# Kernel optimization log

Measured on AMD Instinct MI355X. Metric: run time of the kernel, lower is better.

Reference implementation:

```python
import jax, jax.numpy as jnp
import numpy as np

B, N, HID, EPOCH = 16, 512, 32, 201


def setup_inputs() -> dict:
    key = jax.random.key(0)
    k1, k2, k3, k4 = jax.random.split(key, 4)
    f = jax.random.normal(k1, (B, 1, N, N), dtype=jnp.float32)
    # per-sample 3x3 stencil: perturbed 5-point Laplacian, positive center for stable Jacobi
    base = jnp.array([[0., -1., 0.], [-1., 4., -1.], [0., -1., 0.]], dtype=jnp.float32)
    kernelA = base[None, None] + 0.1 * jax.random.normal(k2, (B, 1, 3, 3), dtype=jnp.float32)
    kernelA = kernelA.at[:, :, 1, 1].set(jnp.maximum(kernelA[:, :, 1, 1], 1.0))
    u = jnp.zeros((B, 1, N, N), jnp.float32)
    # stand-in DeepONet H: pointwise 2 -> HID -> 1 MLP on concat(LFA, residual)
    W1 = 0.1 * jax.random.normal(k3, (HID, 2), dtype=jnp.float32)
    b1 = jnp.zeros((HID,), jnp.float32)
    W2 = 0.1 * jax.random.normal(k4, (1, HID), dtype=jnp.float32)
    b2 = jnp.zeros((1,), jnp.float32)
    return {"f": f, "kernelA": kernelA, "u": u, "W1": W1, "b1": b1, "W2": W2, "b2": b2, "epoch": EPOCH}


def _A(x, kernel):
    # per-sample 3x3 stencil: batch dim mapped to channels, grouped conv (groups = B)
    bsz = x.shape[0]
    y = jax.lax.conv_general_dilated(
        jnp.transpose(x, (1, 0, 2, 3)), kernel, (1, 1), ((1, 1), (1, 1)),
        dimension_numbers=("NCHW", "OIHW", "NCHW"), feature_group_count=bsz)
    return jnp.transpose(y, (1, 0, 2, 3))


def _lfa(kernelA, n):
    # ComputeSmootherFactor: Jacobi symbol |prod_j (1 - tau * A_hat(theta))| on the frequency grid
    h = 1.0 / (n + 1)
    p = np.arange(-(n // 2), n // 2)
    P1, P2 = np.meshgrid(p, p)
    t1 = jnp.asarray(2j * np.pi * h * P1, jnp.complex64)
    t2 = jnp.asarray(2j * np.pi * h * P2, jnp.complex64)
    E = jnp.stack([
        jnp.exp(-t1 - t2), jnp.exp(-t2), jnp.exp(t1 - t2),
        jnp.exp(-t1), jnp.ones_like(t1), jnp.exp(t1),
        jnp.exp(-t1 + t2), jnp.exp(t2), jnp.exp(t1 + t2)])  # [9,N,N]
    bsz = kernelA.shape[0]
    S = jnp.einsum("bk,kxy->bxy", kernelA.reshape(bsz, 9).astype(jnp.complex64), E)
    tau = (0.5 / kernelA[:, 0, 1, 1]).astype(jnp.complex64)[:, None, None]
    y = (1.0 - tau * S) ** 5  # 5 identical Jacobi factors
    return jnp.abs(y)[:, None].astype(jnp.float32)  # [B,1,N,N]


def _H(lfa, r, W1, b1, W2, b2):
    # pointwise MLP correction operator (stand-in for DeepONet)
    z = jnp.concatenate([lfa, r], axis=1)  # [B,2,N,N]
    hdn = jax.nn.gelu(jnp.einsum("bcxy,oc->boxy", z, W1) + b1[None, :, None, None])
    return jnp.einsum("bcxy,oc->boxy", hdn, W2) + b2[None, :, None, None]


def reference(f, kernelA, u, W1, b1, W2, b2, epoch):
    K = (epoch - 1) // 100 + 1
    n = f.shape[-1]
    lfa = _lfa(kernelA, n)
    taus = 0.5 / kernelA[:, :, 1:2, 1:2]  # [B,1,1,1], w=0.5
    x = jnp.zeros_like(f)
    for _ in range(K):
        for _ in range(10):  # jacobi, M=10
            x = x + taus * (f - _A(x, kernelA))
        r = f - _A(x, kernelA)
        x = x + _H(lfa, r, W1, b1, W2, b2)
    r = f - _A(x, kernelA)
    return jnp.linalg.norm(r) / jnp.linalg.norm(f)
```

## Files before the change

kernel.cpp:

```cpp
#include <hip/hip_runtime.h>
#include <math.h>

#define BB 16
#define NN 512
#define HID 32

#define HALO 16
#define TW 96
#define TWP 97
#define OT 64

#define GELU_K1 (-2.302208201f)
#define GELU_K2 (-0.102944244f)

#define TPH 0.012247925f
#define CDR 0.99992499f
#define SDR 0.012247618f

__global__ __launch_bounds__(256) void lfa_kernel(const float* __restrict__ kernelA,
                                                  float* __restrict__ lfa) {
    const int t = threadIdx.x;
    const int strip = t & 127;
    const int i = blockIdx.y * 2 + (t >> 7);
    const int b = blockIdx.z;
    const int j0 = strip * 4;
    const float* a = kernelA + b * 9;
    float a0 = a[0], a1 = a[1], a2 = a[2], a3 = a[3], a4 = a[4];
    float a5 = a[5], a6 = a[6], a7 = a[7], a8 = a[8];
    const float A35 = a3 + a5, A17 = a1 + a7, A08 = a0 + a8, A26 = a2 + a6;
    const float B53 = a5 - a3, B71 = a7 - a1, B80 = a8 - a0, B26 = a2 - a6;
    const float tau = 0.5f / a4;

    float th2 = TPH * (float)(i - NN / 2);
    float th1 = TPH * (float)(j0 - NN / 2);
    float s1, c1, s2, c2;
    sincosf(th1, &s1, &c1);
    sincosf(th2, &s2, &c2);

    float out[4];
#pragma unroll
    for (int k = 0; k < 4; ++k) {
        float cc = c1 * c2, ss = s1 * s2, sc = s1 * c2, cs = c1 * s2;
        float cpp = cc - ss, cpm = cc + ss, spp = sc + cs, spm = sc - cs;
        float re = fmaf(A35, c1, a4); re = fmaf(A17, c2, re);
        re = fmaf(A08, cpp, re);      re = fmaf(A26, cpm, re);
        float im = B53 * s1;          im = fmaf(B71, s2, im);
        im = fmaf(B80, spp, im);      im = fmaf(B26, spm, im);
        float zre = fmaf(-tau, re, 1.0f);
        float zim = tau * im;
        float m2 = fmaf(zre, zre, zim * zim);
        out[k] = m2 * m2 * sqrtf(m2);
        float tt = s1 * SDR;
        float ns = fmaf(s1, CDR, c1 * SDR);
        c1 = fmaf(c1, CDR, -tt);
        s1 = ns;
    }
    float4 ov = {out[0], out[1], out[2], out[3]};
    *(float4*)(lfa + (size_t)b * NN * NN + (size_t)i * NN + j0) = ov;
}

template <bool FIRST>
__global__ __launch_bounds__(256) void fused_cycle(
        const float* __restrict__ xin, float* __restrict__ xout,
        const float* __restrict__ f, const float* __restrict__ kernelA,
        const float* __restrict__ lfa,
        const float* __restrict__ W1, const float* __restrict__ b1,
        const float* __restrict__ W2, const float* __restrict__ b2) {
    __shared__ float sxraw[98 * TWP + 2];
    float* sx = sxraw + TWP + 1;
    const int tx = threadIdx.x;
    const int ty = threadIdx.y;
    const int t  = ty * 32 + tx;
    const int b  = blockIdx.z;
    const int gy0 = blockIdx.y * OT;
    const int gx0 = blockIdx.x * OT;
    const int goi = gy0 - HALO;
    const int goj = gx0 - HALO;
    const float* fg = f + (size_t)b * NN * NN;
    const float* ag = kernelA + b * 9;
    const float ar0 = ag[0], ar1 = ag[1], ar2 = ag[2], ar3 = ag[3], ar4 = ag[4];
    const float ar5 = ag[5], ar6 = ag[6], ar7 = ag[7], ar8 = ag[8];
    const float tau = 0.5f / ar4;
    const float s0 = tau * ar0, q1 = tau * ar1, q2 = tau * ar2, q3 = tau * ar3;
    const float q4 = tau * ar4, q5 = tau * ar5, q6 = tau * ar6, q7 = tau * ar7;
    const float q8 = tau * ar8;

    if (t < 98) sxraw[t] = 0.f;
    if (t < 96) sxraw[97 + 97 * t] = 0.f;
    if (t < 98) sxraw[9409 + t] = 0.f;

    if (!FIRST) {
        const float* xg = xin + (size_t)b * NN * NN;
#pragma unroll
        for (int k = 0; k < (TW * TW) / 256; ++k) {
            int idx = t + k * 256;
            int row = idx / TW, col = idx - row * TW;
            int gi = goi + row, gj = goj + col;
            float v = 0.f;
            if (gi >= 0 && gi < NN && gj >= 0 && gj < NN) v = xg[gi * NN + gj];
            sx[row * TWP + col] = v;
        }
    }

    const int R0 = ty * 12, C0 = tx * 3;

    const float* pb  = sx + (R0 - 1) * TWP + (C0 - 1);
    float*       pwv = sx + R0 * TWP + C0;

    float vR[12], vC[3];
#pragma unroll
    for (int r = 0; r < 12; ++r) {
        int R = R0 + r, gi = goi + R;
        vR[r] = (R >= 1 && R < TW - 1 && gi >= 0 && gi < NN) ? 1.f : 0.f;
    }
#pragma unroll
    for (int c = 0; c < 3; ++c) {
        int C = C0 + c, gj = goj + C;
        vC[c] = (C >= 1 && C < TW - 1 && gj >= 0 && gj < NN) ? 1.f : 0.f;
    }

    float frt[12][3];
#pragma unroll
    for (int r = 0; r < 12; ++r) {
        int gi = goi + R0 + r;
#pragma unroll
        for (int c = 0; c < 3; ++c) {
            int gj = goj + C0 + c;
            frt[r][c] = (gi >= 0 && gi < NN && gj >= 0 && gj < NN)
                            ? tau * fg[gi * NN + gj] : 0.f;
        }
    }

    __syncthreads();

    float cur[12][3];
    if (FIRST) {
#pragma unroll
        for (int r = 0; r < 12; ++r) {
#pragma unroll
            for (int c = 0; c < 3; ++c)
                cur[r][c] = (vR[r] * vC[c]) * frt[r][c];
        }
        pwv[0] = cur[0][0]; pwv[1] = cur[0][1]; pwv[2] = cur[0][2];
        pwv[11 * TWP] = cur[11][0]; pwv[11 * TWP + 1] = cur[11][1];
        pwv[11 * TWP + 2] = cur[11][2];
#pragma unroll
        for (int r = 1; r < 11; ++r) {
            pwv[r * TWP] = cur[r][0];
            pwv[r * TWP + 2] = cur[r][2];
        }
        __syncthreads();
    } else {
#pragma unroll
        for (int r = 0; r < 12; ++r) {
            cur[r][0] = pwv[r * TWP];
            cur[r][1] = pwv[r * TWP + 1];
            cur[r][2] = pwv[r * TWP + 2];
        }
    }

    for (int s = FIRST ? 1 : 0; s < 10; ++s) {
        float top0 = pb[0], top1 = pb[1], top2 = pb[2], top3 = pb[3], top4 = pb[4];
        float bot0 = pb[13 * TWP],     bot1 = pb[13 * TWP + 1],
              bot2 = pb[13 * TWP + 2], bot3 = pb[13 * TWP + 3],
              bot4 = pb[13 * TWP + 4];
        float pm0 = top1, pm1v = top2, pm2 = top3;
        float Lm1 = top0, Rm1 = top4;
        float Lc = pb[TWP], Rc = pb[TWP + 4];
#pragma unroll
        for (int r = 0; r < 12; ++r) {
            float n0, n1, n2, Lp, Rp;
            if (r < 11) {
                n0 = cur[r + 1][0]; n1 = cur[r + 1][1]; n2 = cur[r + 1][2];
                Lp = pb[(r + 2) * TWP];
                Rp = pb[(r + 2) * TWP + 4];
            } else {
                n0 = bot1; n1 = bot2; n2 = bot3; Lp = bot0; Rp = bot4;
            }
            float o0 = cur[r][0], o1 = cur[r][1], o2 = cur[r][2];
            {
                float ax = s0 * Lm1;
                ax = fmaf(q1, pm0, ax); ax = fmaf(q2, pm1v, ax);
                ax = fmaf(q3, Lc, ax);  ax = fmaf(q4, o0, ax);
                ax = fmaf(q5, o1, ax);  ax = fmaf(q6, Lp, ax);
                ax = fmaf(q7, n0, ax);  ax = fmaf(q8, n1, ax);
                cur[r][0] = fmaf(vR[r] * vC[0], frt[r][0] - ax, o0);
            }
            {
                float ax = s0 * pm0;
                ax = fmaf(q1, pm1v, ax); ax = fmaf(q2, pm2, ax);
                ax = fmaf(q3, o0, ax);   ax = fmaf(q4, o1, ax);
                ax = fmaf(q5, o2, ax);   ax = fmaf(q6, n0, ax);
                ax = fmaf(q7, n1, ax);   ax = fmaf(q8, n2, ax);
                cur[r][1] = fmaf(vR[r] * vC[1], frt[r][1] - ax, o1);
            }
            {
                float ax = s0 * pm1v;
                ax = fmaf(q1, pm2, ax); ax = fmaf(q2, Rm1, ax);
                ax = fmaf(q3, o1, ax);  ax = fmaf(q4, o2, ax);
                ax = fmaf(q5, Rc, ax);  ax = fmaf(q6, n1, ax);
                ax = fmaf(q7, n2, ax);  ax = fmaf(q8, Rp, ax);
                cur[r][2] = fmaf(vR[r] * vC[2], frt[r][2] - ax, o2);
            }
            pm0 = o0; pm1v = o1; pm2 = o2;
            Lm1 = Lc; Rm1 = Rc; Lc = Lp; Rc = Rp;
        }
        __syncthreads();
        if (s < 9) {
            pwv[0] = cur[0][0]; pwv[1] = cur[0][1]; pwv[2] = cur[0][2];
            pwv[11 * TWP] = cur[11][0]; pwv[11 * TWP + 1] = cur[11][1];
            pwv[11 * TWP + 2] = cur[11][2];
#pragma unroll
            for (int r = 1; r < 11; ++r) {
                pwv[r * TWP] = cur[r][0];
                pwv[r * TWP + 2] = cur[r][2];
            }
        } else {
#pragma unroll
            for (int r = 0; r < 12; ++r) {
                pwv[r * TWP] = cur[r][0];
                pwv[r * TWP + 1] = cur[r][1];
                pwv[r * TWP + 2] = cur[r][2];
            }
        }
        __syncthreads();
    }

    const int orow = t >> 2;
    const int oseg = t & 3;
    const int Rl = HALO + orow;
    const int Cl0 = HALO + oseg * 16;
    const float* pw = sx + (Rl - 1) * TWP + (Cl0 - 1);
    float w0[18], w1[18], w2[18];
#pragma unroll
    for (int k = 0; k < 18; ++k) {
        w0[k] = pw[k];
        w1[k] = pw[TWP + k];
        w2[k] = pw[2 * TWP + k];
    }
    const int gi = gy0 + orow;
    const int gjb = gx0 + oseg * 16;
    const float4* f4 = (const float4*)(fg + (size_t)gi * NN + gjb);
    const float4* l4 = (const float4*)(lfa + (size_t)b * NN * NN + (size_t)gi * NN + gjb);
    float fv[16], lv[16];
#pragma unroll
    for (int q = 0; q < 4; ++q) {
        float4 fq = f4[q], lq = l4[q];
        fv[q * 4] = fq.x; fv[q * 4 + 1] = fq.y; fv[q * 4 + 2] = fq.z; fv[q * 4 + 3] = fq.w;
        lv[q * 4] = lq.x; lv[q * 4 + 1] = lq.y; lv[q * 4 + 2] = lq.z; lv[q * 4 + 3] = lq.w;
    }
    float rv[16];
#pragma unroll
    for (int k = 0; k < 16; ++k) {
        float ax = ar0 * w0[k];
        ax = fmaf(ar1, w0[k + 1], ax); ax = fmaf(ar2, w0[k + 2], ax);
        ax = fmaf(ar3, w1[k], ax);     ax = fmaf(ar4, w1[k + 1], ax);
        ax = fmaf(ar5, w1[k + 2], ax); ax = fmaf(ar6, w2[k], ax);
        ax = fmaf(ar7, w2[k + 1], ax); ax = fmaf(ar8, w2[k + 2], ax);
        rv[k] = fv[k] - ax;
    }
    float acc[16];
#pragma unroll
    for (int k = 0; k < 16; ++k) acc[k] = 0.f;
    for (int hh = 0; hh < HID; ++hh) {
        float w1a = W1[2 * hh], w1b = W1[2 * hh + 1], bb = b1[hh], wo = W2[hh];
#pragma unroll
        for (int k = 0; k < 16; ++k) {
            float v = fmaf(w1a, lv[k], fmaf(w1b, rv[k], bb));
            float m = v * fmaf(GELU_K2, v * v, GELU_K1);
            float e = __builtin_amdgcn_exp2f(m);
            float g = v * __builtin_amdgcn_rcpf(1.0f + e);
            acc[k] = fmaf(wo, g, acc[k]);
        }
    }
    const float b2v = b2[0];
    float4* xo4 = (float4*)(xout + (size_t)b * NN * NN + (size_t)gi * NN + gjb);
#pragma unroll
    for (int q = 0; q < 4; ++q) {
        float4 ov;
        ov.x = w1[q * 4 + 1] + acc[q * 4] + b2v;
        ov.y = w1[q * 4 + 2] + acc[q * 4 + 1] + b2v;
        ov.z = w1[q * 4 + 3] + acc[q * 4 + 2] + b2v;
        ov.w = w1[q * 4 + 4] + acc[q * 4 + 3] + b2v;
        xo4[q] = ov;
    }
}

__global__ __launch_bounds__(256) void resnorm_kernel(const float* __restrict__ xin,
                                                      const float* __restrict__ f,
                                                      const float* __restrict__ kernelA,
                                                      float* __restrict__ acc) {
    const int total_strips = BB * NN * (NN / 4);
    float rr = 0.f, f2 = 0.f;
    for (int p = blockIdx.x * 256 + threadIdx.x; p < total_strips;
         p += gridDim.x * 256) {
        int b = p >> 16;
        int rem = p & 65535;
        int i = rem >> 7;
        int js = (rem & 127) << 2;
        const float* a = kernelA + b * 9;
        const float* x = xin + (size_t)b * NN * NN;

        float4 up = {0,0,0,0}, mid, dn = {0,0,0,0};
        float upl = 0.f, upr = 0.f, midl = 0.f, midr = 0.f, dnl = 0.f, dnr = 0.f;
        const float* rowm = x + (size_t)i * NN + js;
        mid = *(const float4*)rowm;
        if (js > 0)       midl = rowm[-1];
        if (js + 4 < NN)  midr = rowm[4];
        if (i > 0) {
            const float* rowu = rowm - NN;
            up = *(const float4*)rowu;
            if (js > 0)      upl = rowu[-1];
            if (js + 4 < NN) upr = rowu[4];
        }
        if (i + 1 < NN) {
            const float* rowd = rowm + NN;
            dn = *(const float4*)rowd;
            if (js > 0)      dnl = rowd[-1];
            if (js + 4 < NN) dnr = rowd[4];
        }
        float u[6] = {upl, up.x, up.y, up.z, up.w, upr};
        float m[6] = {midl, mid.x, mid.y, mid.z, mid.w, midr};
        float d[6] = {dnl, dn.x, dn.y, dn.z, dn.w, dnr};
        float4 fq = *(const float4*)(f + (size_t)b * NN * NN + (size_t)i * NN + js);
        float fvv[4] = {fq.x, fq.y, fq.z, fq.w};
#pragma unroll
        for (int c = 0; c < 4; ++c) {
            float ax = a[0] * u[c];
            ax = fmaf(a[1], u[c + 1], ax); ax = fmaf(a[2], u[c + 2], ax);
            ax = fmaf(a[3], m[c], ax);     ax = fmaf(a[4], m[c + 1], ax);
            ax = fmaf(a[5], m[c + 2], ax); ax = fmaf(a[6], d[c], ax);
            ax = fmaf(a[7], d[c + 1], ax); ax = fmaf(a[8], d[c + 2], ax);
            float r = fvv[c] - ax;
            rr = fmaf(r, r, rr);
            f2 = fmaf(fvv[c], fvv[c], f2);
        }
    }
#pragma unroll
    for (int off = 32; off > 0; off >>= 1) {
        rr += __shfl_down(rr, off, 64);
        f2 += __shfl_down(f2, off, 64);
    }
    __shared__ float sr[4], sf[4];
    int wave = threadIdx.x >> 6;
    if ((threadIdx.x & 63) == 0) { sr[wave] = rr; sf[wave] = f2; }
    __syncthreads();
    if (threadIdx.x == 0) {
        atomicAdd(&acc[0], sr[0] + sr[1] + sr[2] + sr[3]);
        atomicAdd(&acc[1], sf[0] + sf[1] + sf[2] + sf[3]);
    }
}

__global__ void finalize_kernel(const float* __restrict__ acc, float* __restrict__ out) {
    out[0] = sqrtf(acc[0] / acc[1]);
}

extern "C" void kernel_launch(void* const* d_in, const int* in_sizes, int n_in,
                              void* d_out, int out_size, void* d_ws, size_t ws_size,
                              hipStream_t stream) {
    const float* f  = (const float*)d_in[0];
    const float* kA = (const float*)d_in[1];
    float*       u  = (float*)d_in[2];
    const float* W1 = (const float*)d_in[3];
    const float* b1 = (const float*)d_in[4];
    const float* W2 = (const float*)d_in[5];
    const float* b2 = (const float*)d_in[6];
    float* out = (float*)d_out;

    char* ws = (char*)d_ws;
    float* acc = (float*)ws;
    float* xB  = (float*)(ws + 256);
    float* lfa = (float*)(ws + 256 + (size_t)BB * NN * NN * 4);

    hipMemsetAsync(acc, 0, 2 * sizeof(float), stream);

    lfa_kernel<<<dim3(1, NN / 2, BB), 256, 0, stream>>>(kA, lfa);

    dim3 jblk(32, 8);
    dim3 jgrd(NN / OT, NN / OT, BB);

    fused_cycle<true><<<jgrd, jblk, 0, stream>>>(u, xB, f, kA, lfa, W1, b1, W2, b2);
    fused_cycle<false><<<jgrd, jblk, 0, stream>>>(xB, u, f, kA, lfa, W1, b1, W2, b2);
    fused_cycle<false><<<jgrd, jblk, 0, stream>>>(u, xB, f, kA, lfa, W1, b1, W2, b2);

    resnorm_kernel<<<2048, 256, 0, stream>>>(xB, f, kA, acc);
    finalize_kernel<<<1, 1, 0, stream>>>(acc, out);
}
```

Baseline: 431.1 us.

## Fuse LFA computation and final residual norm into the cycle kernels

Folds the LFA symbol computation into the first fused cycle kernel, with each block computing its own tile, and zeroes the accumulator there instead of through a memset. The last cycle no longer writes x to global memory. It stages the H correction in shared memory, recomputes it on a one-cell ring of halo points, and computes the final residual and norms in-kernel. This removes the separate LFA, memset and resnorm launches plus a full write and read of x. The cost is redundant MLP work on the ring points, extra barriers, and a launch-bounds hint that may limit registers.

```diff
diff --git a/kernel.cpp b/kernel.cpp
--- a/kernel.cpp
+++ b/kernel.cpp
@@ -17,55 +17,14 @@
 #define CDR 0.99992499f
 #define SDR 0.012247618f
 
-__global__ __launch_bounds__(256) void lfa_kernel(const float* __restrict__ kernelA,
-                                                  float* __restrict__ lfa) {
-    const int t = threadIdx.x;
-    const int strip = t & 127;
-    const int i = blockIdx.y * 2 + (t >> 7);
-    const int b = blockIdx.z;
-    const int j0 = strip * 4;
-    const float* a = kernelA + b * 9;
-    float a0 = a[0], a1 = a[1], a2 = a[2], a3 = a[3], a4 = a[4];
-    float a5 = a[5], a6 = a[6], a7 = a[7], a8 = a[8];
-    const float A35 = a3 + a5, A17 = a1 + a7, A08 = a0 + a8, A26 = a2 + a6;
-    const float B53 = a5 - a3, B71 = a7 - a1, B80 = a8 - a0, B26 = a2 - a6;
-    const float tau = 0.5f / a4;
-
-    float th2 = TPH * (float)(i - NN / 2);
-    float th1 = TPH * (float)(j0 - NN / 2);
-    float s1, c1, s2, c2;
-    sincosf(th1, &s1, &c1);
-    sincosf(th2, &s2, &c2);
-
-    float out[4];
-#pragma unroll
-    for (int k = 0; k < 4; ++k) {
-        float cc = c1 * c2, ss = s1 * s2, sc = s1 * c2, cs = c1 * s2;
-        float cpp = cc - ss, cpm = cc + ss, spp = sc + cs, spm = sc - cs;
-        float re = fmaf(A35, c1, a4); re = fmaf(A17, c2, re);
-        re = fmaf(A08, cpp, re);      re = fmaf(A26, cpm, re);
-        float im = B53 * s1;          im = fmaf(B71, s2, im);
-        im = fmaf(B80, spp, im);      im = fmaf(B26, spm, im);
-        float zre = fmaf(-tau, re, 1.0f);
-        float zim = tau * im;
-        float m2 = fmaf(zre, zre, zim * zim);
-        out[k] = m2 * m2 * sqrtf(m2);
-        float tt = s1 * SDR;
-        float ns = fmaf(s1, CDR, c1 * SDR);
-        c1 = fmaf(c1, CDR, -tt);
-        s1 = ns;
-    }
-    float4 ov = {out[0], out[1], out[2], out[3]};
-    *(float4*)(lfa + (size_t)b * NN * NN + (size_t)i * NN + j0) = ov;
-}
-
-template <bool FIRST>
-__global__ __launch_bounds__(256) void fused_cycle(
+template <bool FIRST, bool RES>
+__global__ __launch_bounds__(256, 4) void fused_cycle(
         const float* __restrict__ xin, float* __restrict__ xout,
         const float* __restrict__ f, const float* __restrict__ kernelA,
-        const float* __restrict__ lfa,
+        float* __restrict__ lfa,
         const float* __restrict__ W1, const float* __restrict__ b1,
-        const float* __restrict__ W2, const float* __restrict__ b2) {
+        const float* __restrict__ W2, const float* __restrict__ b2,
+        float* __restrict__ accp) {
     __shared__ float sxraw[98 * TWP + 2];
     float* sx = sxraw + TWP + 1;
     const int tx = threadIdx.x;
@@ -85,6 +44,48 @@
     const float q4 = tau * ar4, q5 = tau * ar5, q6 = tau * ar6, q7 = tau * ar7;
     const float q8 = tau * ar8;
 
+    if (FIRST) {
+        if (t == 0 && (blockIdx.x | blockIdx.y | blockIdx.z) == 0) {
+            accp[0] = 0.f;
+            accp[1] = 0.f;
+        }
+        const int orw = t >> 2;
+        const int osg = t & 3;
+        const int gi_ = gy0 + orw;
+        const int gj_ = gx0 + osg * 16;
+        const float A35 = ar3 + ar5, A17 = ar1 + ar7, A08 = ar0 + ar8, A26 = ar2 + ar6;
+        const float B53 = ar5 - ar3, B71 = ar7 - ar1, B80 = ar8 - ar0, B26 = ar2 - ar6;
+        float th2 = TPH * (float)(gi_ - NN / 2);
+        float s2v, c2v;
+        sincosf(th2, &s2v, &c2v);
+        float* lrow = lfa + (size_t)b * NN * NN + (size_t)gi_ * NN + gj_;
+        for (int g = 0; g < 4; ++g) {
+            float th1 = TPH * (float)(gj_ + g * 4 - NN / 2);
+            float s1, c1;
+            sincosf(th1, &s1, &c1);
+            float out[4];
+#pragma unroll
+            for (int k = 0; k < 4; ++k) {
+                float cc = c1 * c2v, ss = s1 * s2v, sc = s1 * c2v, cs = c1 * s2v;
+                float cpp = cc - ss, cpm = cc + ss, spp = sc + cs, spm = sc - cs;
+                float re = fmaf(A35, c1, ar4); re = fmaf(A17, c2v, re);
+                re = fmaf(A08, cpp, re);       re = fmaf(A26, cpm, re);
+                float im = B53 * s1;           im = fmaf(B71, s2v, im);
+                im = fmaf(B80, spp, im);       im = fmaf(B26, spm, im);
+                float zre = fmaf(-tau, re, 1.0f);
+                float zim = tau * im;
+                float m2 = fmaf(zre, zre, zim * zim);
+                out[k] = m2 * m2 * sqrtf(m2);
+                float tt = s1 * SDR;
+                float ns = fmaf(s1, CDR, c1 * SDR);
+                c1 = fmaf(c1, CDR, -tt);
+                s1 = ns;
+            }
+            float4 ov = {out[0], out[1], out[2], out[3]};
+            *(float4*)(lrow + g * 4) = ov;
+        }
+    }
+
     if (t < 98) sxraw[t] = 0.f;
     if (t < 96) sxraw[97 + 97 * t] = 0.f;
     if (t < 98) sxraw[9409 + t] = 0.f;
@@ -259,6 +260,12 @@
         ax = fmaf(ar7, w2[k + 1], ax); ax = fmaf(ar8, w2[k + 2], ax);
         rv[k] = fv[k] - ax;
     }
+    float f2 = 0.f;
+    if (RES) {
+#pragma unroll
+        for (int k = 0; k < 16; ++k) f2 = fmaf(fv[k], fv[k], f2);
+    }
+    const float b2v = b2[0];
     float acc[16];
 #pragma unroll
     for (int k = 0; k < 16; ++k) acc[k] = 0.f;
@@ -273,81 +280,106 @@
             acc[k] = fmaf(wo, g, acc[k]);
         }
     }
-    const float b2v = b2[0];
-    float4* xo4 = (float4*)(xout + (size_t)b * NN * NN + (size_t)gi * NN + gjb);
-#pragma unroll
-    for (int q = 0; q < 4; ++q) {
-        float4 ov;
-        ov.x = w1[q * 4 + 1] + acc[q * 4] + b2v;
-        ov.y = w1[q * 4 + 2] + acc[q * 4 + 1] + b2v;
-        ov.z = w1[q * 4 + 3] + acc[q * 4 + 2] + b2v;
-        ov.w = w1[q * 4 + 4] + acc[q * 4 + 3] + b2v;
-        xo4[q] = ov;
-    }
-}
-
-__global__ __launch_bounds__(256) void resnorm_kernel(const float* __restrict__ xin,
-                                                      const float* __restrict__ f,
-                                                      const float* __restrict__ kernelA,
-                                                      float* __restrict__ acc) {
-    const int total_strips = BB * NN * (NN / 4);
-    float rr = 0.f, f2 = 0.f;
-    for (int p = blockIdx.x * 256 + threadIdx.x; p < total_strips;
-         p += gridDim.x * 256) {
-        int b = p >> 16;
-        int rem = p & 65535;
-        int i = rem >> 7;
-        int js = (rem & 127) << 2;
-        const float* a = kernelA + b * 9;
-        const float* x = xin + (size_t)b * NN * NN;
-
-        float4 up = {0,0,0,0}, mid, dn = {0,0,0,0};
-        float upl = 0.f, upr = 0.f, midl = 0.f, midr = 0.f, dnl = 0.f, dnr = 0.f;
-        const float* rowm = x + (size_t)i * NN + js;
-        mid = *(const float4*)rowm;
-        if (js > 0)       midl = rowm[-1];
-        if (js + 4 < NN)  midr = rowm[4];
-        if (i > 0) {
-            const float* rowu = rowm - NN;
-            up = *(const float4*)rowu;
-            if (js > 0)      upl = rowu[-1];
-            if (js + 4 < NN) upr = rowu[4];
-        }
-        if (i + 1 < NN) {
-            const float* rowd = rowm + NN;
-            dn = *(const float4*)rowd;
-            if (js > 0)      dnl = rowd[-1];
-            if (js + 4 < NN) dnr = rowd[4];
-        }
-        float u[6] = {upl, up.x, up.y, up.z, up.w, upr};
-        float m[6] = {midl, mid.x, mid.y, mid.z, mid.w, midr};
-        float d[6] = {dnl, dn.x, dn.y, dn.z, dn.w, dnr};
-        float4 fq = *(const float4*)(f + (size_t)b * NN * NN + (size_t)i * NN + js);
-        float fvv[4] = {fq.x, fq.y, fq.z, fq.w};
-#pragma unroll
-        for (int c = 0; c < 4; ++c) {
-            float ax = a[0] * u[c];
-            ax = fmaf(a[1], u[c + 1], ax); ax = fmaf(a[2], u[c + 2], ax);
-            ax = fmaf(a[3], m[c], ax);     ax = fmaf(a[4], m[c + 1], ax);
-            ax = fmaf(a[5], m[c + 2], ax); ax = fmaf(a[6], d[c], ax);
-            ax = fmaf(a[7], d[c + 1], ax); ax = fmaf(a[8], d[c + 2], ax);
-            float r = fvv[c] - ax;
+
+    if (RES) {
+        float Hr0 = 0.f, Hr1 = 0.f;
+        int hoff0 = 0, hoff1 = 0;
+        auto ringH = [&](int rc, float& Hv, int& hoff) {
+            int R, C;
+            if (rc < 66)       { R = 15; C = 15 + rc; }
+            else if (rc < 132) { R = 80; C = rc - 51; }
+            else if (rc < 196) { R = rc - 116; C = 15; }
+            else               { R = rc - 180; C = 80; }
+            hoff = R * TWP + C;
+            int rgi = goi + R, rgj = goj + C;
+            Hv = 0.f;
+            if (rgi >= 0 && rgi < NN && rgj >= 0 && rgj < NN) {
+                const float* pr = sx + (R - 1) * TWP + (C - 1);
+                float u0 = pr[0], u1 = pr[1], u2 = pr[2];
+                float m0 = pr[TWP], m1 = pr[TWP + 1], m2 = pr[TWP + 2];
+                float d0 = pr[2 * TWP], d1 = pr[2 * TWP + 1], d2 = pr[2 * TWP + 2];
+                float ax = ar0 * u0;
+                ax = fmaf(ar1, u1, ax); ax = fmaf(ar2, u2, ax);
+                ax = fmaf(ar3, m0, ax); ax = fmaf(ar4, m1, ax);
+                ax = fmaf(ar5, m2, ax); ax = fmaf(ar6, d0, ax);
+                ax = fmaf(ar7, d1, ax); ax = fmaf(ar8, d2, ax);
+                float rp = fg[(size_t)rgi * NN + rgj] - ax;
+                float lf = lfa[(size_t)b * NN * NN + (size_t)rgi * NN + rgj];
+                float av = 0.f;
+                for (int hh = 0; hh < HID; ++hh) {
+                    float w1a = W1[2 * hh], w1b = W1[2 * hh + 1], bbv = b1[hh], wo = W2[hh];
+                    float v = fmaf(w1a, lf, fmaf(w1b, rp, bbv));
+                    float m = v * fmaf(GELU_K2, v * v, GELU_K1);
+                    float e = __builtin_amdgcn_exp2f(m);
+                    float gg = v * __builtin_amdgcn_rcpf(1.0f + e);
+                    av = fmaf(wo, gg, av);
+                }
+                Hv = av + b2v;
+            }
+        };
+        ringH(t, Hr0, hoff0);
+        if (t < 4) ringH(t + 256, Hr1, hoff1);
+
+        __syncthreads();
+        float* ph = sx + Rl * TWP + Cl0;
+#pragma unroll
+        for (int k = 0; k < 16; ++k) ph[k] = acc[k] + b2v;
+        sx[hoff0] = Hr0;
+        if (t < 4) sx[hoff1] = Hr1;
+        __syncthreads();
+
+        float hr[18];
+#pragma unroll
+        for (int k = 0; k < 18; ++k) hr[k] = pw[k];
+#pragma unroll
+        for (int k = 0; k < 16; ++k) {
+            float ax = ar0 * hr[k];
+            ax = fmaf(ar1, hr[k + 1], ax);
+            ax = fmaf(ar2, hr[k + 2], ax);
+            rv[k] -= ax;
+        }
+#pragma unroll
+        for (int k = 0; k < 18; ++k) hr[k] = pw[TWP + k];
+#pragma unroll
+        for (int k = 0; k < 16; ++k) {
+            float ax = ar3 * hr[k];
+            ax = fmaf(ar4, hr[k + 1], ax);
+            ax = fmaf(ar5, hr[k + 2], ax);
+            rv[k] -= ax;
+        }
+#pragma unroll
+        for (int k = 0; k < 18; ++k) hr[k] = pw[2 * TWP + k];
+        float rr = 0.f;
+#pragma unroll
+        for (int k = 0; k < 16; ++k) {
+            float ax = ar6 * hr[k];
+            ax = fmaf(ar7, hr[k + 1], ax);
+            ax = fmaf(ar8, hr[k + 2], ax);
+            float r = rv[k] - ax;
             rr = fmaf(r, r, rr);
-            f2 = fmaf(fvv[c], fvv[c], f2);
-        }
-    }
-#pragma unroll
-    for (int off = 32; off > 0; off >>= 1) {
-        rr += __shfl_down(rr, off, 64);
-        f2 += __shfl_down(f2, off, 64);
-    }
-    __shared__ float sr[4], sf[4];
-    int wave = threadIdx.x >> 6;
-    if ((threadIdx.x & 63) == 0) { sr[wave] = rr; sf[wave] = f2; }
-    __syncthreads();
-    if (threadIdx.x == 0) {
-        atomicAdd(&acc[0], sr[0] + sr[1] + sr[2] + sr[3]);
-        atomicAdd(&acc[1], sf[0] + sf[1] + sf[2] + sf[3]);
+        }
+#pragma unroll
+        for (int off = 32; off > 0; off >>= 1) {
+            rr += __shfl_down(rr, off, 64);
+            f2 += __shfl_down(f2, off, 64);
+        }
+        if ((t & 63) == 0) { sxraw[t >> 6] = rr; sxraw[4 + (t >> 6)] = f2; }
+        __syncthreads();
+        if (t == 0) {
+            atomicAdd(&accp[0], sxraw[0] + sxraw[1] + sxraw[2] + sxraw[3]);
+            atomicAdd(&accp[1], sxraw[4] + sxraw[5] + sxraw[6] + sxraw[7]);
+        }
+    } else {
+        float4* xo4 = (float4*)(xout + (size_t)b * NN * NN + (size_t)gi * NN + gjb);
+#pragma unroll
+        for (int q = 0; q < 4; ++q) {
+            float4 ov;
+            ov.x = w1[q * 4 + 1] + acc[q * 4] + b2v;
+            ov.y = w1[q * 4 + 2] + acc[q * 4 + 1] + b2v;
+            ov.z = w1[q * 4 + 3] + acc[q * 4 + 2] + b2v;
+            ov.w = w1[q * 4 + 4] + acc[q * 4 + 3] + b2v;
+            xo4[q] = ov;
+        }
     }
 }
 
@@ -372,17 +404,12 @@
     float* xB  = (float*)(ws + 256);
     float* lfa = (float*)(ws + 256 + (size_t)BB * NN * NN * 4);
 
-    hipMemsetAsync(acc, 0, 2 * sizeof(float), stream);
-
-    lfa_kernel<<<dim3(1, NN / 2, BB), 256, 0, stream>>>(kA, lfa);
-
     dim3 jblk(32, 8);
     dim3 jgrd(NN / OT, NN / OT, BB);
 
-    fused_cycle<true><<<jgrd, jblk, 0, stream>>>(u, xB, f, kA, lfa, W1, b1, W2, b2);
-    fused_cycle<false><<<jgrd, jblk, 0, stream>>>(xB, u, f, kA, lfa, W1, b1, W2, b2);
-    fused_cycle<false><<<jgrd, jblk, 0, stream>>>(u, xB, f, kA, lfa, W1, b1, W2, b2);
-
-    resnorm_kernel<<<2048, 256, 0, stream>>>(xB, f, kA, acc);
+    fused_cycle<true,  false><<<jgrd, jblk, 0, stream>>>(u, xB, f, kA, lfa, W1, b1, W2, b2, acc);
+    fused_cycle<false, false><<<jgrd, jblk, 0, stream>>>(xB, u, f, kA, lfa, W1, b1, W2, b2, acc);
+    fused_cycle<false, true ><<<jgrd, jblk, 0, stream>>>(u, xB, f, kA, lfa, W1, b1, W2, b2, acc);
+
     finalize_kernel<<<1, 1, 0, stream>>>(acc, out);
 }
```

Result: slower. 582.1 us (+35.0%).
